# Kernel optimization log

Hardware: AMD Instinct MI355X
Metric: run time of the kernel (lower is better)

Reference implementation:

```python
import jax, jax.numpy as jnp
import numpy as np

IMG_FEAT = 2048
HIDDEN = 1024
K_TIMES = 3
GLIMPSE = 8
BA_HIDDEN = K_TIMES * HIDDEN  # 3072


def setup_inputs() -> dict:
    key = jax.random.key(0)
    ks = jax.random.split(key, 9)
    b, n_v, n_q = 64, 128, 32
    v = jax.random.normal(ks[0], (b, n_v, IMG_FEAT), dtype=jnp.float32)
    q = jax.random.normal(ks[1], (b, n_q, HIDDEN), dtype=jnp.float32)
    # weight-normed Linear params (weight_norm with dim=None -> scalar g)
    v_w = jax.random.normal(ks[2], (BA_HIDDEN, IMG_FEAT), dtype=jnp.float32) * 0.02
    v_g = jnp.asarray(jnp.linalg.norm(v_w), dtype=jnp.float32)
    v_b = jnp.zeros((BA_HIDDEN,), dtype=jnp.float32)
    q_w = jax.random.normal(ks[3], (BA_HIDDEN, HIDDEN), dtype=jnp.float32) * 0.02
    q_g = jnp.asarray(jnp.linalg.norm(q_w), dtype=jnp.float32)
    q_b = jnp.zeros((BA_HIDDEN,), dtype=jnp.float32)
    h_mat = jax.random.normal(ks[4], (1, GLIMPSE, 1, BA_HIDDEN), dtype=jnp.float32)
    h_bias = jax.random.normal(ks[5], (1, GLIMPSE, 1, 1), dtype=jnp.float32)
    return {"v": v, "q": q, "v_w": v_w, "v_g": v_g, "v_b": v_b,
            "q_w": q_w, "q_g": q_g, "q_b": q_b,
            "h_mat": h_mat, "h_bias": h_bias}


def _wn_linear_relu(x, w, g, b):
    # weight_norm(dim=None): w_eff = g * w / ||w||_F (scalar g)
    w_eff = (g / jnp.linalg.norm(w)) * w
    return jax.nn.relu(jnp.einsum('bnd,kd->bnk', x, w_eff) + b)


def reference(v, q, v_w, v_g, v_b, q_w, q_g, q_b, h_mat, h_bias):
    # dropout layers are identity in eval mode
    v_ = _wn_linear_relu(v, v_w, v_g, v_b)  # [b, n_v, K]
    q_ = _wn_linear_relu(q, q_w, q_g, q_b)  # [b, n_q, K]
    # einsum('xhyk,bvk,bqk->bhvq') with h_mat [1,g,1,K]
    hm = h_mat[0, :, 0, :]  # [g, K]
    logits = jnp.einsum('hk,bvk,bqk->bhvq', hm, v_, q_) + h_bias
    return logits
```

## Files before the change

kernel.cpp:

```cpp
#include <hip/hip_runtime.h>

typedef __attribute__((ext_vector_type(8))) __bf16 bf16x8;
typedef __attribute__((ext_vector_type(4))) float f32x4;
typedef const __attribute__((address_space(1))) unsigned int gas_u32;
typedef __attribute__((address_space(3))) unsigned int las_u32;

__device__ __forceinline__ unsigned short f2bf(float f) {
  unsigned u = __builtin_bit_cast(unsigned, f);
  u = (u + 0x7FFFu + ((u >> 16) & 1u)) >> 16;
  return (unsigned short)u;
}
__device__ __forceinline__ float bf2f(unsigned short h) {
  return __builtin_bit_cast(float, (unsigned)h << 16);
}

__global__ __launch_bounds__(256) void k_cvt(const float* __restrict__ in,
                                             unsigned short* __restrict__ out, int n8) {
  for (int i = blockIdx.x * 256 + threadIdx.x; i < n8; i += gridDim.x * 256) {
    float4 a = ((const float4*)in)[2 * i];
    float4 b = ((const float4*)in)[2 * i + 1];
    uint4 o;
    o.x = f2bf(a.x) | ((unsigned)f2bf(a.y) << 16);
    o.y = f2bf(a.z) | ((unsigned)f2bf(a.w) << 16);
    o.z = f2bf(b.x) | ((unsigned)f2bf(b.y) << 16);
    o.w = f2bf(b.z) | ((unsigned)f2bf(b.w) << 16);
    ((uint4*)out)[i] = o;
  }
}

__global__ __launch_bounds__(256) void k_cvt_sq(const float* __restrict__ in,
                                                unsigned short* __restrict__ out, int n8,
                                                float* __restrict__ ssout) {
  int tid = threadIdx.x;
  float s = 0.f;
  for (int i = blockIdx.x * 256 + tid; i < n8; i += gridDim.x * 256) {
    float4 a = ((const float4*)in)[2 * i];
    float4 b = ((const float4*)in)[2 * i + 1];
    s += a.x * a.x + a.y * a.y + a.z * a.z + a.w * a.w;
    s += b.x * b.x + b.y * b.y + b.z * b.z + b.w * b.w;
    uint4 o;
    o.x = f2bf(a.x) | ((unsigned)f2bf(a.y) << 16);
    o.y = f2bf(a.z) | ((unsigned)f2bf(a.w) << 16);
    o.z = f2bf(b.x) | ((unsigned)f2bf(b.y) << 16);
    o.w = f2bf(b.z) | ((unsigned)f2bf(b.w) << 16);
    ((uint4*)out)[i] = o;
  }
  for (int off = 32; off; off >>= 1) s += __shfl_down(s, off);
  __shared__ float red[4];
  if ((tid & 63) == 0) red[tid >> 6] = s;
  __syncthreads();
  if (tid == 0) atomicAdd(ssout, red[0] + red[1] + red[2] + red[3]);
}

__global__ __launch_bounds__(512, 2) void k_gemm_wn(
    const unsigned short* __restrict__ A, const unsigned short* __restrict__ B,
    const float* __restrict__ bias, const float* __restrict__ gptr,
    const float* __restrict__ ssptr, unsigned short* __restrict__ C,
    int M, int N, int K, int nbm) {
  __shared__ __align__(16) unsigned short lA[2 * 128 * 64];
  __shared__ __align__(16) unsigned short lB[2 * 384 * 64];
  const int tid = threadIdx.x;
  const int wid = tid >> 6, lane = tid & 63;
  const int l15 = lane & 15, l4 = lane >> 4;
  const int wm = wid >> 2, wn = wid & 3;
  const int rr = tid >> 3;
  const int scol = ((tid & 7) ^ (rr & 7)) << 3;

  int nwg = gridDim.x;
  int wg = (blockIdx.x & 7) * (nwg >> 3) + (blockIdx.x >> 3);
  int bm = wg % nbm, bn = wg / nbm;

  const unsigned short* Ab = A + (size_t)bm * 128 * K;
  const unsigned short* Bb = B + (size_t)bn * 384 * K;
  const int nt = K >> 6;

#define STAGEU(U, TS)                                                            \
  {                                                                              \
    int ts_ = (TS) < nt ? (TS) : nt - 1;                                         \
    if ((U) < 2) {                                                               \
      __builtin_amdgcn_global_load_lds(                                          \
          (gas_u32*)(Ab + (size_t)((U)*64 + rr) * K + ts_ * 64 + scol),          \
          (las_u32*)(lA + ((TS)&1) * 8192 + (U)*4096 + tid * 8), 16, 0, 0);      \
    } else {                                                                     \
      __builtin_amdgcn_global_load_lds(                                          \
          (gas_u32*)(Bb + (size_t)(((U)-2) * 64 + rr) * K + ts_ * 64 + scol),    \
          (las_u32*)(lB + ((TS)&1) * 24576 + ((U)-2) * 4096 + tid * 8), 16, 0,   \
          0);                                                                    \
    }                                                                            \
  }

#define LDSA(DST, MQ, TP)                                                        \
  _Pragma("unroll") for (int i2 = 0; i2 < 2; ++i2) {                             \
    int rl = wm * 64 + ((MQ)*2 + i2) * 16 + l15;                                 \
    const unsigned short* ap = lA + (TP)*8192 + rl * 64;                         \
    int s8 = rl & 7;                                                             \
    DST[i2][0] = *(const bf16x8*)(ap + ((l4 ^ s8) << 3));                        \
    DST[i2][1] = *(const bf16x8*)(ap + (((4 | l4) ^ s8) << 3));                  \
  }

#define LDSB(DST, NQ, TP)                                                        \
  _Pragma("unroll") for (int j3 = 0; j3 < 3; ++j3) {                             \
    int rl = wn * 96 + ((NQ)*3 + j3) * 16 + l15;                                 \
    const unsigned short* bp = lB + (TP)*24576 + rl * 64;                        \
    int s8 = rl & 7;                                                             \
    DST[j3][0] = *(const bf16x8*)(bp + ((l4 ^ s8) << 3));                        \
    DST[j3][1] = *(const bf16x8*)(bp + (((4 | l4) ^ s8) << 3));                  \
  }

#define MFMA12(MQ, NQ, AF, BF)                                                   \
  _Pragma("unroll") for (int ks = 0; ks < 2; ++ks)                               \
  _Pragma("unroll") for (int i2 = 0; i2 < 2; ++i2)                               \
  _Pragma("unroll") for (int j3 = 0; j3 < 3; ++j3)                               \
    acc[(MQ)*2 + i2][(NQ)*3 + j3] = __builtin_amdgcn_mfma_f32_16x16x32_bf16(     \
        AF[i2][ks], BF[j3][ks], acc[(MQ)*2 + i2][(NQ)*3 + j3], 0, 0, 0);

  f32x4 acc[4][6] = {};
  bf16x8 a0_[2][2], a1_[2][2], b0_[3][2], b1_[3][2];

  STAGEU(0, 0) STAGEU(1, 0) STAGEU(2, 0) STAGEU(3, 0)
  STAGEU(4, 0) STAGEU(5, 0) STAGEU(6, 0) STAGEU(7, 0)
  STAGEU(0, 1) STAGEU(1, 1)
  asm volatile("s_waitcnt vmcnt(2)" ::: "memory");
  __builtin_amdgcn_sched_barrier(0);
  __builtin_amdgcn_s_barrier();
  LDSA(a0_, 0, 0)
  STAGEU(2, 1) STAGEU(3, 1) STAGEU(6, 1) STAGEU(7, 1)
  LDSB(b0_, 0, 0)

  for (int t = 0; t < nt; ++t) {
    const int cp = t & 1, np = (t + 1) & 1;
    LDSB(b1_, 1, cp)
    STAGEU(4, t + 1) STAGEU(5, t + 1)
    __builtin_amdgcn_s_setprio(1);
    MFMA12(0, 0, a0_, b0_)
    __builtin_amdgcn_s_setprio(0);
    LDSA(a1_, 1, cp)
    __builtin_amdgcn_s_setprio(1);
    MFMA12(0, 1, a0_, b1_)
    __builtin_amdgcn_s_setprio(0);
    asm volatile("s_waitcnt lgkmcnt(0)" ::: "memory");
    asm volatile("s_waitcnt vmcnt(6)" ::: "memory");
    __builtin_amdgcn_sched_barrier(0);
    __builtin_amdgcn_s_barrier();
    LDSA(a0_, 0, np)
    STAGEU(0, t + 2) STAGEU(1, t + 2)
    __builtin_amdgcn_s_setprio(1);
    MFMA12(1, 0, a1_, b0_)
    __builtin_amdgcn_s_setprio(0);
    asm volatile("s_waitcnt vmcnt(2)" ::: "memory");
    __builtin_amdgcn_sched_barrier(0);
    __builtin_amdgcn_s_barrier();
    LDSB(b0_, 0, np)
    STAGEU(2, t + 2) STAGEU(3, t + 2) STAGEU(6, t + 2) STAGEU(7, t + 2)
    __builtin_amdgcn_s_setprio(1);
    MFMA12(1, 1, a1_, b1_)
    __builtin_amdgcn_s_setprio(0);
  }

  asm volatile("s_waitcnt vmcnt(0)" ::: "memory");

  float s = gptr[0] / sqrtf(ssptr[0]);
#pragma unroll
  for (int nj = 0; nj < 6; ++nj) {
    int gcol = bn * 384 + wn * 96 + nj * 16 + l15;
    float bv = bias[gcol];
#pragma unroll
    for (int mi = 0; mi < 4; ++mi) {
#pragma unroll
      for (int r = 0; r < 4; ++r) {
        int grow = bm * 128 + wm * 64 + mi * 16 + l4 * 4 + r;
        float v = fmaxf(acc[mi][nj][r] * s + bv, 0.f);
        C[(size_t)grow * N + gcol] = f2bf(v);
      }
    }
  }
#undef STAGEU
#undef LDSA
#undef LDSB
#undef MFMA12
}

__global__ __launch_bounds__(256, 2) void k_gemm_bt(
    const unsigned short* __restrict__ A, const unsigned short* __restrict__ B,
    const float* __restrict__ bias, const float* __restrict__ gptr,
    const float* __restrict__ ssptr, unsigned short* __restrict__ C,
    int M, int N, int K, int nbm) {
  __shared__ __align__(16) unsigned short lA[128 * 64];
  __shared__ __align__(16) unsigned short lB[128 * 64];
  int tid = threadIdx.x;
  int wid = tid >> 6, lane = tid & 63;
  int l15 = lane & 15, l4 = lane >> 4;
  int w0 = wid >> 1, w1 = wid & 1;

  int nwg = gridDim.x;
  int wg = (blockIdx.x & 7) * (nwg >> 3) + (blockIdx.x >> 3);
  int bm = wg % nbm, bn = wg / nbm;

  const unsigned short* Ab = A + (size_t)bm * 128 * K;
  const unsigned short* Bb = B + (size_t)bn * 128 * K;

  f32x4 acc[4][4] = {};

  for (int k0 = 0; k0 < K; k0 += 64) {
    __syncthreads();
#pragma unroll
    for (int i = 0; i < 4; ++i) {
      int ebase = (i * 4 + wid) << 9;
      int eoff = ebase + lane * 8;
      int row = eoff >> 6, col = eoff & 63;
      __builtin_amdgcn_global_load_lds(
          (gas_u32*)(Ab + (size_t)row * K + k0 + col),
          (las_u32*)(lA + ebase), 16, 0, 0);
      __builtin_amdgcn_global_load_lds(
          (gas_u32*)(Bb + (size_t)row * K + k0 + col),
          (las_u32*)(lB + ebase), 16, 0, 0);
    }
    __syncthreads();
#pragma unroll
    for (int ks = 0; ks < 2; ++ks) {
      bf16x8 af[4], bfr[4];
#pragma unroll
      for (int mi = 0; mi < 4; ++mi)
        af[mi] = *(const bf16x8*)(lA + ((w0 * 64 + mi * 16 + l15) * 64 + ks * 32 + l4 * 8));
#pragma unroll
      for (int nj = 0; nj < 4; ++nj)
        bfr[nj] = *(const bf16x8*)(lB + ((w1 * 64 + nj * 16 + l15) * 64 + ks * 32 + l4 * 8));
#pragma unroll
      for (int mi = 0; mi < 4; ++mi)
#pragma unroll
        for (int nj = 0; nj < 4; ++nj)
          acc[mi][nj] =
              __builtin_amdgcn_mfma_f32_16x16x32_bf16(af[mi], bfr[nj], acc[mi][nj], 0, 0, 0);
    }
  }

  float s = gptr[0] / sqrtf(ssptr[0]);
#pragma unroll
  for (int mi = 0; mi < 4; ++mi)
#pragma unroll
    for (int nj = 0; nj < 4; ++nj) {
      int col = bn * 128 + w1 * 64 + nj * 16 + l15;
      float bv = bias[col];
#pragma unroll
      for (int r = 0; r < 4; ++r) {
        int row = bm * 128 + w0 * 64 + mi * 16 + l4 * 4 + r;
        float v = fmaxf(acc[mi][nj][r] * s + bv, 0.f);
        C[(size_t)row * N + col] = f2bf(v);
      }
    }
}

__global__ __launch_bounds__(256, 2) void k_glimpse3(
    const unsigned short* __restrict__ Vh, const unsigned short* __restrict__ Qh,
    const float* __restrict__ hmat, const float* __restrict__ hbias,
    float* __restrict__ out) {
  __shared__ __align__(16) unsigned short lV[3][128 * 64];
  __shared__ __align__(16) unsigned short lQ[2][2][32 * 64];
  int tid = threadIdx.x;
  int wid = tid >> 6, lane = tid & 63;
  int l15 = lane & 15, l4 = lane >> 4;

  int id = blockIdx.x;
  int b = id & 63, h2 = id >> 6;

  const unsigned short* Vb = Vh + (size_t)b * 128 * 3072;
  const unsigned short* Qb = Qh + (size_t)b * 32 * 3072;
  const float* hr0 = hmat + h2 * 3072;
  const float* hr1 = hmat + (h2 + 4) * 3072;

  f32x4 acc[2][2][2] = {};
  int eoff = tid * 8;
  int qr = eoff >> 6, qc = eoff & 63;
  const int NT = 48;

#define VSTAGE(T, SLOT)                                                          \
  {                                                                              \
    int tc = (T) < NT ? (T) : NT - 1;                                            \
    _Pragma("unroll") for (int i = 0; i < 4; ++i) {                              \
      int ebase = (i * 4 + wid) << 9;                                            \
      int eo = ebase + lane * 8;                                                 \
      int row = eo >> 6, col = eo & 63;                                          \
      __builtin_amdgcn_global_load_lds(                                          \
          (gas_u32*)(Vb + (size_t)row * 3072 + tc * 64 + col),                   \
          (las_u32*)(&lV[SLOT][0] + ebase), 16, 0, 0);                           \
    }                                                                            \
  }

#define QLOAD(T, RQ, H0A, H0B, H1A, H1B)                                         \
  {                                                                              \
    int tc = (T) < NT ? (T) : NT - 1;                                            \
    RQ = *(const uint4*)(Qb + (size_t)qr * 3072 + tc * 64 + qc);                 \
    const float* hp0 = hr0 + tc * 64 + qc;                                       \
    const float* hp1 = hr1 + tc * 64 + qc;                                       \
    H0A = ((const float4*)hp0)[0];                                               \
    H0B = ((const float4*)hp0)[1];                                               \
    H1A = ((const float4*)hp1)[0];                                               \
    H1B = ((const float4*)hp1)[1];                                               \
  }

#define QWRITE(CB, RQ, H0A, H0B, H1A, H1B)                                       \
  {                                                                              \
    float e0 = bf2f((unsigned short)(RQ.x & 0xffff));                            \
    float e1 = bf2f((unsigned short)(RQ.x >> 16));                               \
    float e2 = bf2f((unsigned short)(RQ.y & 0xffff));                            \
    float e3 = bf2f((unsigned short)(RQ.y >> 16));                               \
    float e4 = bf2f((unsigned short)(RQ.z & 0xffff));                            \
    float e5 = bf2f((unsigned short)(RQ.z >> 16));                               \
    float e6 = bf2f((unsigned short)(RQ.w & 0xffff));                            \
    float e7 = bf2f((unsigned short)(RQ.w >> 16));                               \
    uint4 o0, o1;                                                                \
    o0.x = f2bf(e0 * H0A.x) | ((unsigned)f2bf(e1 * H0A.y) << 16);                \
    o0.y = f2bf(e2 * H0A.z) | ((unsigned)f2bf(e3 * H0A.w) << 16);                \
    o0.z = f2bf(e4 * H0B.x) | ((unsigned)f2bf(e5 * H0B.y) << 16);                \
    o0.w = f2bf(e6 * H0B.z) | ((unsigned)f2bf(e7 * H0B.w) << 16);                \
    o1.x = f2bf(e0 * H1A.x) | ((unsigned)f2bf(e1 * H1A.y) << 16);                \
    o1.y = f2bf(e2 * H1A.z) | ((unsigned)f2bf(e3 * H1A.w) << 16);                \
    o1.z = f2bf(e4 * H1B.x) | ((unsigned)f2bf(e5 * H1B.y) << 16);                \
    o1.w = f2bf(e6 * H1B.z) | ((unsigned)f2bf(e7 * H1B.w) << 16);                \
    *(uint4*)(&lQ[CB][0][0] + eoff) = o0;                                        \
    *(uint4*)(&lQ[CB][1][0] + eoff) = o1;                                        \
  }

#define GMFMA(SLOT, CB)                                                          \
  _Pragma("unroll") for (int ks = 0; ks < 2; ++ks) {                             \
    bf16x8 af[2];                                                                \
    _Pragma("unroll") for (int mi = 0; mi < 2; ++mi)                             \
      af[mi] = *(const bf16x8*)(&lV[SLOT][0] +                                   \
                                ((wid * 32 + mi * 16 + l15) * 64 + ks * 32 + l4 * 8)); \
    _Pragma("unroll") for (int hh = 0; hh < 2; ++hh) {                           \
      bf16x8 bq[2];                                                              \
      _Pragma("unroll") for (int nj = 0; nj < 2; ++nj)                           \
        bq[nj] = *(const bf16x8*)(&lQ[CB][hh][0] +                               \
                                  ((nj * 16 + l15) * 64 + ks * 32 + l4 * 8));    \
      _Pragma("unroll") for (int mi = 0; mi < 2; ++mi)                           \
        _Pragma("unroll") for (int nj = 0; nj < 2; ++nj)                         \
          acc[hh][mi][nj] = __builtin_amdgcn_mfma_f32_16x16x32_bf16(             \
              af[mi], bq[nj], acc[hh][mi][nj], 0, 0, 0);                         \
    }                                                                            \
  }

#define GBODY(T, CQ, CH0A, CH0B, CH1A, CH1B, NQ, NH0A, NH0B, NH1A, NH1B)         \
  {                                                                              \
    QLOAD((T) + 2, NQ, NH0A, NH0B, NH1A, NH1B)                                   \
    asm volatile("s_waitcnt vmcnt(9)" ::: "memory");                             \
    asm volatile("s_waitcnt lgkmcnt(0)" ::: "memory");                           \
    __builtin_amdgcn_sched_barrier(0);                                           \
    __builtin_amdgcn_s_barrier();                                                \
    VSTAGE((T) + 2, ((T) + 2) % 3)                                               \
    QWRITE(((T) + 1) & 1, CQ, CH0A, CH0B, CH1A, CH1B)                            \
    GMFMA((T) % 3, (T) & 1)                                                      \
  }

  uint4 aq, bq_;
  float4 ah0a, ah0b, ah1a, ah1b, bh0a, bh0b, bh1a, bh1b;

  QLOAD(0, aq, ah0a, ah0b, ah1a, ah1b)
  QLOAD(1, bq_, bh0a, bh0b, bh1a, bh1b)
  VSTAGE(0, 0)
  VSTAGE(1, 1)
  asm volatile("s_waitcnt vmcnt(13)" ::: "memory");
  __builtin_amdgcn_sched_barrier(0);
  QWRITE(0, aq, ah0a, ah0b, ah1a, ah1b)

  for (int t = 0; t < NT; t += 2) {
    GBODY(t, bq_, bh0a, bh0b, bh1a, bh1b, aq, ah0a, ah0b, ah1a, ah1b)
    GBODY(t + 1, aq, ah0a, ah0b, ah1a, ah1b, bq_, bh0a, bh0b, bh1a, bh1b)
  }
  asm volatile("s_waitcnt vmcnt(0) lgkmcnt(0)" ::: "memory");

#pragma unroll
  for (int hh = 0; hh < 2; ++hh) {
    int h = h2 + hh * 4;
    float hb = hbias[h];
    float* ob = out + (size_t)(b * 8 + h) * 128 * 32;
#pragma unroll
    for (int mi = 0; mi < 2; ++mi)
#pragma unroll
      for (int nj = 0; nj < 2; ++nj)
#pragma unroll
        for (int r = 0; r < 4; ++r) {
          int row = wid * 32 + mi * 16 + l4 * 4 + r;
          int col = nj * 16 + l15;
          ob[row * 32 + col] = acc[hh][mi][nj][r] + hb;
        }
  }
#undef VSTAGE
#undef QLOAD
#undef QWRITE
#undef GMFMA
#undef GBODY
}

extern "C" void kernel_launch(void* const* d_in, const int* in_sizes, int n_in,
                              void* d_out, int out_size, void* d_ws, size_t ws_size,
                              hipStream_t stream) {
  const float* v = (const float*)d_in[0];
  const float* q = (const float*)d_in[1];
  const float* v_w = (const float*)d_in[2];
  const float* v_g = (const float*)d_in[3];
  const float* v_b = (const float*)d_in[4];
  const float* q_w = (const float*)d_in[5];
  const float* q_g = (const float*)d_in[6];
  const float* q_b = (const float*)d_in[7];
  const float* hmat = (const float*)d_in[8];
  const float* hbias = (const float*)d_in[9];
  float* out = (float*)d_out;

  const size_t n_v = 16777216;
  const size_t n_vw = 6291456;
  const size_t n_q = 2097152;
  const size_t n_qw = 3145728;
  const size_t n_vh = 25165824;
  const size_t n_qh = 6291456;

  char* ws = (char*)d_ws;
  float* ss = (float*)ws;
  size_t off = 256;
  unsigned short* v_bf = (unsigned short*)(ws + off);  off += n_v * 2;
  unsigned short* vw_bf = (unsigned short*)(ws + off); off += n_vw * 2;
  unsigned short* q_bf = (unsigned short*)(ws + off);  off += n_q * 2;
  unsigned short* qw_bf = (unsigned short*)(ws + off); off += n_qw * 2;
  unsigned short* v_h = (unsigned short*)(ws + off);   off += n_vh * 2;
  unsigned short* q_h = (unsigned short*)(ws + off);   off += n_qh * 2;

  (void)hipMemsetAsync(ss, 0, 8, stream);
  k_cvt_sq<<<512, 256, 0, stream>>>(v_w, vw_bf, (int)(n_vw / 8), ss + 0);
  k_cvt_sq<<<512, 256, 0, stream>>>(q_w, qw_bf, (int)(n_qw / 8), ss + 1);
  k_cvt<<<1024, 256, 0, stream>>>(v, v_bf, (int)(n_v / 8));
  k_cvt<<<1024, 256, 0, stream>>>(q, q_bf, (int)(n_q / 8));

  k_gemm_wn<<<512, 512, 0, stream>>>(v_bf, vw_bf, v_b, v_g, ss + 0, v_h,
                                     8192, 3072, 2048, 64);
  k_gemm_bt<<<384, 256, 0, stream>>>(q_bf, qw_bf, q_b, q_g, ss + 1, q_h,
                                     2048, 3072, 1024, 16);

  k_glimpse3<<<256, 256, 0, stream>>>(v_h, q_h, hmat, hbias, out);
}
```

Measured before the change: 236.4 us.

## Fuse conversion kernels, remap GEMM tiles, add sched barriers, widen glimpse heads

Merges the four fp32-to-bf16 conversion launches into one k_prep kernel that partitions blocks across inputs, which cuts launch overhead and runs them concurrently. Swaps the v-GEMM workgroup mapping to row-major over N tiles and inserts sched_barriers between LDS reads, global stages and MFMA groups to fix instruction ordering. The glimpse kernel now computes four heads per block instead of two, halving the grid to 128 blocks. Each Q/V tile is reused across more heads, but there is less parallelism and more register and LDS pressure.

```diff
diff --git a/kernel.cpp b/kernel.cpp
--- a/kernel.cpp
+++ b/kernel.cpp
@@ -14,11 +14,35 @@
   return __builtin_bit_cast(float, (unsigned)h << 16);
 }
 
-__global__ __launch_bounds__(256) void k_cvt(const float* __restrict__ in,
-                                             unsigned short* __restrict__ out, int n8) {
-  for (int i = blockIdx.x * 256 + threadIdx.x; i < n8; i += gridDim.x * 256) {
+__global__ __launch_bounds__(256) void k_prep(
+    const float* __restrict__ v, const float* __restrict__ q,
+    const float* __restrict__ vw, const float* __restrict__ qw,
+    unsigned short* __restrict__ v_bf, unsigned short* __restrict__ q_bf,
+    unsigned short* __restrict__ vw_bf, unsigned short* __restrict__ qw_bf,
+    float* __restrict__ ss) {
+  __shared__ float red[4];
+  int bid = blockIdx.x, tid = threadIdx.x;
+  const float* in;
+  unsigned short* out;
+  float* ssout = nullptr;
+  int n8, b0, nb;
+  if (bid < 768) {
+    in = v; out = v_bf; n8 = 2097152; b0 = bid; nb = 768;
+  } else if (bid < 864) {
+    in = q; out = q_bf; n8 = 262144; b0 = bid - 768; nb = 96;
+  } else if (bid < 1344) {
+    in = vw; out = vw_bf; n8 = 786432; b0 = bid - 864; nb = 480; ssout = ss + 0;
+  } else {
+    in = qw; out = qw_bf; n8 = 393216; b0 = bid - 1344; nb = 192; ssout = ss + 1;
+  }
+  float s = 0.f;
+  for (int i = b0 * 256 + tid; i < n8; i += nb * 256) {
     float4 a = ((const float4*)in)[2 * i];
     float4 b = ((const float4*)in)[2 * i + 1];
+    if (ssout) {
+      s += a.x * a.x + a.y * a.y + a.z * a.z + a.w * a.w;
+      s += b.x * b.x + b.y * b.y + b.z * b.z + b.w * b.w;
+    }
     uint4 o;
     o.x = f2bf(a.x) | ((unsigned)f2bf(a.y) << 16);
     o.y = f2bf(a.z) | ((unsigned)f2bf(a.w) << 16);
@@ -26,37 +50,19 @@
     o.w = f2bf(b.z) | ((unsigned)f2bf(b.w) << 16);
     ((uint4*)out)[i] = o;
   }
-}
-
-__global__ __launch_bounds__(256) void k_cvt_sq(const float* __restrict__ in,
-                                                unsigned short* __restrict__ out, int n8,
-                                                float* __restrict__ ssout) {
-  int tid = threadIdx.x;
-  float s = 0.f;
-  for (int i = blockIdx.x * 256 + tid; i < n8; i += gridDim.x * 256) {
-    float4 a = ((const float4*)in)[2 * i];
-    float4 b = ((const float4*)in)[2 * i + 1];
-    s += a.x * a.x + a.y * a.y + a.z * a.z + a.w * a.w;
-    s += b.x * b.x + b.y * b.y + b.z * b.z + b.w * b.w;
-    uint4 o;
-    o.x = f2bf(a.x) | ((unsigned)f2bf(a.y) << 16);
-    o.y = f2bf(a.z) | ((unsigned)f2bf(a.w) << 16);
-    o.z = f2bf(b.x) | ((unsigned)f2bf(b.y) << 16);
-    o.w = f2bf(b.z) | ((unsigned)f2bf(b.w) << 16);
-    ((uint4*)out)[i] = o;
-  }
-  for (int off = 32; off; off >>= 1) s += __shfl_down(s, off);
-  __shared__ float red[4];
-  if ((tid & 63) == 0) red[tid >> 6] = s;
-  __syncthreads();
-  if (tid == 0) atomicAdd(ssout, red[0] + red[1] + red[2] + red[3]);
+  if (ssout) {
+    for (int off = 32; off; off >>= 1) s += __shfl_down(s, off);
+    if ((tid & 63) == 0) red[tid >> 6] = s;
+    __syncthreads();
+    if (tid == 0) atomicAdd(ssout, red[0] + red[1] + red[2] + red[3]);
+  }
 }
 
 __global__ __launch_bounds__(512, 2) void k_gemm_wn(
     const unsigned short* __restrict__ A, const unsigned short* __restrict__ B,
     const float* __restrict__ bias, const float* __restrict__ gptr,
     const float* __restrict__ ssptr, unsigned short* __restrict__ C,
-    int M, int N, int K, int nbm) {
+    int M, int N, int K, int nbn) {
   __shared__ __align__(16) unsigned short lA[2 * 128 * 64];
   __shared__ __align__(16) unsigned short lB[2 * 384 * 64];
   const int tid = threadIdx.x;
@@ -68,11 +74,13 @@
 
   int nwg = gridDim.x;
   int wg = (blockIdx.x & 7) * (nwg >> 3) + (blockIdx.x >> 3);
-  int bm = wg % nbm, bn = wg / nbm;
+  int bm = wg / nbn, bn = wg % nbn;
 
   const unsigned short* Ab = A + (size_t)bm * 128 * K;
   const unsigned short* Bb = B + (size_t)bn * 384 * K;
   const int nt = K >> 6;
+
+#define SB() __builtin_amdgcn_sched_barrier(0);
 
 #define STAGEU(U, TS)                                                            \
   {                                                                              \
@@ -121,37 +129,47 @@
   STAGEU(4, 0) STAGEU(5, 0) STAGEU(6, 0) STAGEU(7, 0)
   STAGEU(0, 1) STAGEU(1, 1)
   asm volatile("s_waitcnt vmcnt(2)" ::: "memory");
-  __builtin_amdgcn_sched_barrier(0);
+  SB()
   __builtin_amdgcn_s_barrier();
   LDSA(a0_, 0, 0)
+  SB()
   STAGEU(2, 1) STAGEU(3, 1) STAGEU(6, 1) STAGEU(7, 1)
+  SB()
   LDSB(b0_, 0, 0)
+  SB()
 
   for (int t = 0; t < nt; ++t) {
     const int cp = t & 1, np = (t + 1) & 1;
     LDSB(b1_, 1, cp)
+    SB()
     STAGEU(4, t + 1) STAGEU(5, t + 1)
+    SB()
     __builtin_amdgcn_s_setprio(1);
     MFMA12(0, 0, a0_, b0_)
     __builtin_amdgcn_s_setprio(0);
     LDSA(a1_, 1, cp)
+    SB()
     __builtin_amdgcn_s_setprio(1);
     MFMA12(0, 1, a0_, b1_)
     __builtin_amdgcn_s_setprio(0);
     asm volatile("s_waitcnt lgkmcnt(0)" ::: "memory");
     asm volatile("s_waitcnt vmcnt(6)" ::: "memory");
-    __builtin_amdgcn_sched_barrier(0);
+    SB()
     __builtin_amdgcn_s_barrier();
     LDSA(a0_, 0, np)
+    SB()
     STAGEU(0, t + 2) STAGEU(1, t + 2)
+    SB()
     __builtin_amdgcn_s_setprio(1);
     MFMA12(1, 0, a1_, b0_)
     __builtin_amdgcn_s_setprio(0);
     asm volatile("s_waitcnt vmcnt(2)" ::: "memory");
-    __builtin_amdgcn_sched_barrier(0);
+    SB()
     __builtin_amdgcn_s_barrier();
     LDSB(b0_, 0, np)
+    SB()
     STAGEU(2, t + 2) STAGEU(3, t + 2) STAGEU(6, t + 2) STAGEU(7, t + 2)
+    SB()
     __builtin_amdgcn_s_setprio(1);
     MFMA12(1, 1, a1_, b1_)
     __builtin_amdgcn_s_setprio(0);
@@ -178,6 +196,7 @@
 #undef LDSA
 #undef LDSB
 #undef MFMA12
+#undef SB
 }
 
 __global__ __launch_bounds__(256, 2) void k_gemm_bt(
@@ -250,25 +269,27 @@
     }
 }
 
-__global__ __launch_bounds__(256, 2) void k_glimpse3(
+__global__ __launch_bounds__(256, 2) void k_glimpse4(
     const unsigned short* __restrict__ Vh, const unsigned short* __restrict__ Qh,
     const float* __restrict__ hmat, const float* __restrict__ hbias,
     float* __restrict__ out) {
   __shared__ __align__(16) unsigned short lV[3][128 * 64];
-  __shared__ __align__(16) unsigned short lQ[2][2][32 * 64];
+  __shared__ __align__(16) unsigned short lQ[2][4][32 * 64];
   int tid = threadIdx.x;
   int wid = tid >> 6, lane = tid & 63;
   int l15 = lane & 15, l4 = lane >> 4;
 
   int id = blockIdx.x;
-  int b = id & 63, h2 = id >> 6;
+  int b = id & 63, h4 = id >> 6;
 
   const unsigned short* Vb = Vh + (size_t)b * 128 * 3072;
   const unsigned short* Qb = Qh + (size_t)b * 32 * 3072;
-  const float* hr0 = hmat + h2 * 3072;
-  const float* hr1 = hmat + (h2 + 4) * 3072;
-
-  f32x4 acc[2][2][2] = {};
+  const float* hr0 = hmat + (h4 * 4 + 0) * 3072;
+  const float* hr1 = hmat + (h4 * 4 + 1) * 3072;
+  const float* hr2 = hmat + (h4 * 4 + 2) * 3072;
+  const float* hr3 = hmat + (h4 * 4 + 3) * 3072;
+
+  f32x4 acc[4][2][2] = {};
   int eoff = tid * 8;
   int qr = eoff >> 6, qc = eoff & 63;
   const int NT = 48;
@@ -286,19 +307,21 @@
     }                                                                            \
   }
 
-#define QLOAD(T, RQ, H0A, H0B, H1A, H1B)                                         \
+#define QLOAD(T, RQ, H)                                                          \
   {                                                                              \
     int tc = (T) < NT ? (T) : NT - 1;                                            \
     RQ = *(const uint4*)(Qb + (size_t)qr * 3072 + tc * 64 + qc);                 \
-    const float* hp0 = hr0 + tc * 64 + qc;                                       \
-    const float* hp1 = hr1 + tc * 64 + qc;                                       \
-    H0A = ((const float4*)hp0)[0];                                               \
-    H0B = ((const float4*)hp0)[1];                                               \
-    H1A = ((const float4*)hp1)[0];                                               \
-    H1B = ((const float4*)hp1)[1];                                               \
-  }
-
-#define QWRITE(CB, RQ, H0A, H0B, H1A, H1B)                                       \
+    H[0] = ((const float4*)(hr0 + tc * 64 + qc))[0];                             \
+    H[1] = ((const float4*)(hr0 + tc * 64 + qc))[1];                             \
+    H[2] = ((const float4*)(hr1 + tc * 64 + qc))[0];                             \
+    H[3] = ((const float4*)(hr1 + tc * 64 + qc))[1];                             \
+    H[4] = ((const float4*)(hr2 + tc * 64 + qc))[0];                             \
+    H[5] = ((const float4*)(hr2 + tc * 64 + qc))[1];                             \
+    H[6] = ((const float4*)(hr3 + tc * 64 + qc))[0];                             \
+    H[7] = ((const float4*)(hr3 + tc * 64 + qc))[1];                             \
+  }
+
+#define QWRITE(CB, RQ, H)                                                        \
   {                                                                              \
     float e0 = bf2f((unsigned short)(RQ.x & 0xffff));                            \
     float e1 = bf2f((unsigned short)(RQ.x >> 16));                               \
@@ -308,17 +331,16 @@
     float e5 = bf2f((unsigned short)(RQ.z >> 16));                               \
     float e6 = bf2f((unsigned short)(RQ.w & 0xffff));                            \
     float e7 = bf2f((unsigned short)(RQ.w >> 16));                               \
-    uint4 o0, o1;                                                                \
-    o0.x = f2bf(e0 * H0A.x) | ((unsigned)f2bf(e1 * H0A.y) << 16);                \
-    o0.y = f2bf(e2 * H0A.z) | ((unsigned)f2bf(e3 * H0A.w) << 16);                \
-    o0.z = f2bf(e4 * H0B.x) | ((unsigned)f2bf(e5 * H0B.y) << 16);                \
-    o0.w = f2bf(e6 * H0B.z) | ((unsigned)f2bf(e7 * H0B.w) << 16);                \
-    o1.x = f2bf(e0 * H1A.x) | ((unsigned)f2bf(e1 * H1A.y) << 16);                \
-    o1.y = f2bf(e2 * H1A.z) | ((unsigned)f2bf(e3 * H1A.w) << 16);                \
-    o1.z = f2bf(e4 * H1B.x) | ((unsigned)f2bf(e5 * H1B.y) << 16);                \
-    o1.w = f2bf(e6 * H1B.z) | ((unsigned)f2bf(e7 * H1B.w) << 16);                \
-    *(uint4*)(&lQ[CB][0][0] + eoff) = o0;                                        \
-    *(uint4*)(&lQ[CB][1][0] + eoff) = o1;                                        \
+    _Pragma("unroll") for (int hh = 0; hh < 4; ++hh) {                           \
+      uint4 o;                                                                   \
+      o.x = f2bf(e0 * H[hh * 2].x) | ((unsigned)f2bf(e1 * H[hh * 2].y) << 16);   \
+      o.y = f2bf(e2 * H[hh * 2].z) | ((unsigned)f2bf(e3 * H[hh * 2].w) << 16);   \
+      o.z = f2bf(e4 * H[hh * 2 + 1].x) |                                         \
+            ((unsigned)f2bf(e5 * H[hh * 2 + 1].y) << 16);                        \
+      o.w = f2bf(e6 * H[hh * 2 + 1].z) |                                         \
+            ((unsigned)f2bf(e7 * H[hh * 2 + 1].w) << 16);                        \
+      *(uint4*)(&lQ[CB][hh][0] + eoff) = o;                                      \
+    }                                                                            \
   }
 
 #define GMFMA(SLOT, CB)                                                          \
@@ -327,7 +349,7 @@
     _Pragma("unroll") for (int mi = 0; mi < 2; ++mi)                             \
       af[mi] = *(const bf16x8*)(&lV[SLOT][0] +                                   \
                                 ((wid * 32 + mi * 16 + l15) * 64 + ks * 32 + l4 * 8)); \
-    _Pragma("unroll") for (int hh = 0; hh < 2; ++hh) {                           \
+    _Pragma("unroll") for (int hh = 0; hh < 4; ++hh) {                           \
       bf16x8 bq[2];                                                              \
       _Pragma("unroll") for (int nj = 0; nj < 2; ++nj)                           \
         bq[nj] = *(const bf16x8*)(&lQ[CB][hh][0] +                               \
@@ -339,38 +361,38 @@
     }                                                                            \
   }
 
-#define GBODY(T, CQ, CH0A, CH0B, CH1A, CH1B, NQ, NH0A, NH0B, NH1A, NH1B)         \
+#define GBODY(T, CQ, CH, NQ, NH)                                                 \
   {                                                                              \
-    QLOAD((T) + 2, NQ, NH0A, NH0B, NH1A, NH1B)                                   \
-    asm volatile("s_waitcnt vmcnt(9)" ::: "memory");                             \
+    QLOAD((T) + 2, NQ, NH)                                                       \
+    asm volatile("s_waitcnt vmcnt(13)" ::: "memory");                            \
     asm volatile("s_waitcnt lgkmcnt(0)" ::: "memory");                           \
     __builtin_amdgcn_sched_barrier(0);                                           \
     __builtin_amdgcn_s_barrier();                                                \
     VSTAGE((T) + 2, ((T) + 2) % 3)                                               \
-    QWRITE(((T) + 1) & 1, CQ, CH0A, CH0B, CH1A, CH1B)                            \
+    QWRITE(((T) + 1) & 1, CQ, CH)                                                \
     GMFMA((T) % 3, (T) & 1)                                                      \
   }
 
   uint4 aq, bq_;
-  float4 ah0a, ah0b, ah1a, ah1b, bh0a, bh0b, bh1a, bh1b;
-
-  QLOAD(0, aq, ah0a, ah0b, ah1a, ah1b)
-  QLOAD(1, bq_, bh0a, bh0b, bh1a, bh1b)
+  float4 ah[8], bh[8];
+
+  QLOAD(0, aq, ah)
+  QLOAD(1, bq_, bh)
   VSTAGE(0, 0)
   VSTAGE(1, 1)
-  asm volatile("s_waitcnt vmcnt(13)" ::: "memory");
+  asm volatile("s_waitcnt vmcnt(17)" ::: "memory");
   __builtin_amdgcn_sched_barrier(0);
-  QWRITE(0, aq, ah0a, ah0b, ah1a, ah1b)
+  QWRITE(0, aq, ah)
 
   for (int t = 0; t < NT; t += 2) {
-    GBODY(t, bq_, bh0a, bh0b, bh1a, bh1b, aq, ah0a, ah0b, ah1a, ah1b)
-    GBODY(t + 1, aq, ah0a, ah0b, ah1a, ah1b, bq_, bh0a, bh0b, bh1a, bh1b)
+    GBODY(t, bq_, bh, aq, ah)
+    GBODY(t + 1, aq, ah, bq_, bh)
   }
   asm volatile("s_waitcnt vmcnt(0) lgkmcnt(0)" ::: "memory");
 
 #pragma unroll
-  for (int hh = 0; hh < 2; ++hh) {
-    int h = h2 + hh * 4;
+  for (int hh = 0; hh < 4; ++hh) {
+    int h = h4 * 4 + hh;
     float hb = hbias[h];
     float* ob = out + (size_t)(b * 8 + h) * 128 * 32;
 #pragma unroll
@@ -424,15 +446,12 @@
   unsigned short* q_h = (unsigned short*)(ws + off);   off += n_qh * 2;
 
   (void)hipMemsetAsync(ss, 0, 8, stream);
-  k_cvt_sq<<<512, 256, 0, stream>>>(v_w, vw_bf, (int)(n_vw / 8), ss + 0);
-  k_cvt_sq<<<512, 256, 0, stream>>>(q_w, qw_bf, (int)(n_qw / 8), ss + 1);
-  k_cvt<<<1024, 256, 0, stream>>>(v, v_bf, (int)(n_v / 8));
-  k_cvt<<<1024, 256, 0, stream>>>(q, q_bf, (int)(n_q / 8));
+  k_prep<<<1536, 256, 0, stream>>>(v, q, v_w, q_w, v_bf, q_bf, vw_bf, qw_bf, ss);
 
   k_gemm_wn<<<512, 512, 0, stream>>>(v_bf, vw_bf, v_b, v_g, ss + 0, v_h,
-                                     8192, 3072, 2048, 64);
+                                     8192, 3072, 2048, 8);
   k_gemm_bt<<<384, 256, 0, stream>>>(q_bf, qw_bf, q_b, q_g, ss + 1, q_h,
                                      2048, 3072, 1024, 16);
 
-  k_glimpse3<<<256, 256, 0, stream>>>(v_h, q_h, hmat, hbias, out);
-}
+  k_glimpse4<<<128, 256, 0, stream>>>(v_h, q_h, hmat, hbias, out);
+}
```

Measured after the change: 240.0 us. No clear change (+1.5%).
